# Kernel tuning notes

Measured on AMD Instinct MI355X. Metric: run time of the kernel, lower is better.

Reference implementation:

```python
import jax, jax.numpy as jnp
import numpy as np

K = 16            # number of instance labels (static; labels are 0..K-1)
DELTA_V = 0.2     # delta_variance_loss
DELTA_D = 0.2     # delta_cluster_distance
ALPHA, BETA, GAMMA = 1.0, 1.0, 0.001


def _safe_sqrt(x):
    # sqrt with zero (not nan) gradient at x == 0
    pos = x > 0
    return jnp.where(pos, jnp.sqrt(jnp.where(pos, x, 1.0)), 0.0)


def setup_inputs() -> dict:
    key = jax.random.key(0)
    k1, k2 = jax.random.split(key)
    features = jax.random.normal(k1, (4, 32, 256, 512), dtype=jnp.float32)
    ground_truth = jax.random.randint(k2, (4, 256, 512), 0, K, dtype=jnp.int64)
    return {"features": features, "ground_truth": ground_truth}


def reference(features, ground_truth):
    N, C, H, W = features.shape
    P = H * W
    feat = features.reshape(N, C, P)                  # (N,C,P)
    gt = ground_truth.reshape(N, P)                   # (N,P)
    onehot = (gt[:, :, None] == jnp.arange(K)[None, None, :]).astype(feat.dtype)  # (N,P,K)

    # cluster mean: torch.mean(feature * mask, dim=1) -> masked sum / (H*W)  (faithful quirk)
    mu = jnp.einsum('ncp,npk->nck', feat, onehot) / P  # (N,C,K)

    # ---- variance loss ----
    # per pixel p, instance k: || feat[:,p]*mask_pk - mu[:,k] ||_2 over channels.
    # expand: mask*(||f||^2 - 2 f.mu) + ||mu||^2   (mask in {0,1} so mask^2 = mask)
    sq_f = jnp.sum(feat * feat, axis=1)               # (N,P)
    dot = jnp.einsum('ncp,nck->npk', feat, mu)        # (N,P,K)
    sq_mu = jnp.sum(mu * mu, axis=1)                  # (N,K)
    sq = onehot * (sq_f[:, :, None] - 2.0 * dot) + sq_mu[:, None, :]  # (N,P,K)
    d = _safe_sqrt(jnp.maximum(sq, 0.0))
    v = jnp.mean(d, axis=1)                           # (N,K) mean over pixels
    variance_loss = jnp.mean(jnp.mean(jnp.maximum(v - DELTA_V, 0.0), axis=1))

    # ---- distance loss ----
    gram = jnp.einsum('nck,ncj->nkj', mu, mu)         # (N,K,K)
    sqd = sq_mu[:, :, None] + sq_mu[:, None, :] - 2.0 * gram
    eye = jnp.eye(K, dtype=bool)
    D = jnp.where(eye, 0.0, _safe_sqrt(jnp.maximum(jnp.where(eye, 1.0, sqd), 0.0)))
    mean_dist = jnp.sum(D, axis=2) / (K - 1)          # mean over the K-1 other clusters
    distance_loss = jnp.sum(jnp.maximum(2.0 * DELTA_D - mean_dist, 0.0)) / (N * K)

    # ---- normalization loss ----
    normalization_loss = jnp.mean(jnp.mean(_safe_sqrt(sq_mu), axis=1))

    total_loss = ALPHA * variance_loss + BETA * distance_loss + GAMMA * normalization_loss
    return total_loss, variance_loss, distance_loss, normalization_loss, mu
```

## Files before the change

kernel.cpp:

```cpp
#include <hip/hip_runtime.h>
#include <hip/hip_bf16.h>

#define NIMG 4
#define CCH  32
#define PPIX 131072
#define KLBL 16

#define CPB  4
#define NCG  (CCH / CPB)
#define K1_CHUNK 8192
#define K1_NCHUNK (PPIX / K1_CHUNK)
#define K2_CHUNK 1024
#define K2_NCHUNK (PPIX / K2_CHUNK)


__device__ __forceinline__ float wave_sum(float v) {
#pragma unroll
    for (int m = 1; m < 64; m <<= 1) v += __shfl_xor(v, m);
    return v;
}

__global__ __launch_bounds__(256) void k1_mu(const float* __restrict__ feat,
                                             const int* __restrict__ gt,
                                             float* __restrict__ mu_part) {
    int b     = blockIdx.x;
    int chunk = b % K1_NCHUNK;
    int cg    = (b / K1_NCHUNK) % NCG;
    int n     = b / (K1_NCHUNK * NCG);
    int p0    = chunk * K1_CHUNK;
    int tid   = threadIdx.x;

    const float* f0 = feat + ((size_t)(n * CCH + cg * CPB)) * PPIX + p0;
    const float* f1 = f0 + PPIX;
    const float* f2 = f0 + 2 * (size_t)PPIX;
    const float* f3 = f0 + 3 * (size_t)PPIX;
    const int*   g  = gt + (size_t)n * PPIX + p0;

    float acc0[KLBL], acc1[KLBL], acc2[KLBL], acc3[KLBL];
#pragma unroll
    for (int k = 0; k < KLBL; k++) { acc0[k] = 0.f; acc1[k] = 0.f; acc2[k] = 0.f; acc3[k] = 0.f; }

    for (int i = tid * 4; i < K1_CHUNK; i += 256 * 4) {
        float4 a0 = *(const float4*)(f0 + i);
        float4 a1 = *(const float4*)(f1 + i);
        float4 a2 = *(const float4*)(f2 + i);
        float4 a3 = *(const float4*)(f3 + i);
        int4   l  = *(const int4*)(g + i);
#pragma unroll
        for (int k = 0; k < KLBL; k++) {
            float mx = (l.x == k) ? 1.f : 0.f;
            float my = (l.y == k) ? 1.f : 0.f;
            float mz = (l.z == k) ? 1.f : 0.f;
            float mw = (l.w == k) ? 1.f : 0.f;
            acc0[k] = fmaf(a0.x, mx, acc0[k]); acc0[k] = fmaf(a0.y, my, acc0[k]);
            acc0[k] = fmaf(a0.z, mz, acc0[k]); acc0[k] = fmaf(a0.w, mw, acc0[k]);
            acc1[k] = fmaf(a1.x, mx, acc1[k]); acc1[k] = fmaf(a1.y, my, acc1[k]);
            acc1[k] = fmaf(a1.z, mz, acc1[k]); acc1[k] = fmaf(a1.w, mw, acc1[k]);
            acc2[k] = fmaf(a2.x, mx, acc2[k]); acc2[k] = fmaf(a2.y, my, acc2[k]);
            acc2[k] = fmaf(a2.z, mz, acc2[k]); acc2[k] = fmaf(a2.w, mw, acc2[k]);
            acc3[k] = fmaf(a3.x, mx, acc3[k]); acc3[k] = fmaf(a3.y, my, acc3[k]);
            acc3[k] = fmaf(a3.z, mz, acc3[k]); acc3[k] = fmaf(a3.w, mw, acc3[k]);
        }
    }

    __shared__ float warr[4][64];
    int wave = tid >> 6, lane = tid & 63;
#pragma unroll
    for (int k = 0; k < KLBL; k++) {
        float s0 = wave_sum(acc0[k]);
        float s1 = wave_sum(acc1[k]);
        float s2 = wave_sum(acc2[k]);
        float s3 = wave_sum(acc3[k]);
        if (lane == 0) {
            warr[wave][k]      = s0;
            warr[wave][16 + k] = s1;
            warr[wave][32 + k] = s2;
            warr[wave][48 + k] = s3;
        }
    }
    __syncthreads();
    if (tid < 64) {
        float t = warr[0][tid] + warr[1][tid] + warr[2][tid] + warr[3][tid];
        mu_part[(((size_t)n * K1_NCHUNK + chunk) * NCG + cg) * 64 + tid] = t;
    }
}

__global__ __launch_bounds__(256) void k2_var(const float* __restrict__ feat,
                                              const int* __restrict__ gt,
                                              const float* __restrict__ mu_part,
                                              float* __restrict__ sumd_part,
                                              float* __restrict__ cnt_part) {
    __shared__ float lmu[CCH * KLBL];
    int b     = blockIdx.x;
    int chunk = b % K2_NCHUNK;
    int n     = b / K2_NCHUNK;
    int p0    = chunk * K2_CHUNK;
    int tid   = threadIdx.x;
    const float inv_p = 1.0f / (float)PPIX;

    for (int e = tid; e < CCH * KLBL; e += 256) {
        float s = 0.f;
#pragma unroll
        for (int ch = 0; ch < K1_NCHUNK; ch++)
            s += mu_part[(((size_t)n * K1_NCHUNK + ch) * NCG + (e >> 6)) * 64 + (e & 63)];
        lmu[e] = s * inv_p;
    }
    __syncthreads();

    int p = p0 + tid * 4;
    int4 l = *(const int4*)(gt + (size_t)n * PPIX + p);
    float d2x = 0.f, d2y = 0.f, d2z = 0.f, d2w = 0.f;
    const float* fb = feat + (size_t)n * CCH * PPIX + p;
#pragma unroll 8
    for (int c = 0; c < CCH; c++) {
        float4 f = *(const float4*)(fb + (size_t)c * PPIX);
        float mx = lmu[c * KLBL + l.x];
        float my = lmu[c * KLBL + l.y];
        float mz = lmu[c * KLBL + l.z];
        float mw = lmu[c * KLBL + l.w];
        float ex = f.x - mx, ey = f.y - my, ez = f.z - mz, ew = f.w - mw;
        d2x = fmaf(ex, ex, d2x); d2y = fmaf(ey, ey, d2y);
        d2z = fmaf(ez, ez, d2z); d2w = fmaf(ew, ew, d2w);
    }
    float dx = sqrtf(d2x), dy = sqrtf(d2y), dz = sqrtf(d2z), dw = sqrtf(d2w);

    float s[KLBL], ct[KLBL];
#pragma unroll
    for (int k = 0; k < KLBL; k++) {
        float mx = (l.x == k) ? 1.f : 0.f;
        float my = (l.y == k) ? 1.f : 0.f;
        float mz = (l.z == k) ? 1.f : 0.f;
        float mw = (l.w == k) ? 1.f : 0.f;
        s[k]  = fmaf(dx, mx, fmaf(dy, my, fmaf(dz, mz, dw * mw)));
        ct[k] = mx + my + mz + mw;
    }

    __shared__ float warr[4][32];
    int wave = tid >> 6, lane = tid & 63;
#pragma unroll
    for (int k = 0; k < KLBL; k++) {
        float ssum = wave_sum(s[k]);
        float csum = wave_sum(ct[k]);
        if (lane == 0) { warr[wave][k] = ssum; warr[wave][16 + k] = csum; }
    }
    __syncthreads();
    if (tid < 32) {
        float t = warr[0][tid] + warr[1][tid] + warr[2][tid] + warr[3][tid];
        if (tid < 16) sumd_part[(size_t)b * 16 + tid]        = t;
        else          cnt_part [(size_t)b * 16 + (tid - 16)] = t;
    }
}

__global__ __launch_bounds__(256) void k3_final(const float* __restrict__ mu_part,
                                                const float* __restrict__ sumd_part,
                                                const float* __restrict__ cnt_part,
                                                float* __restrict__ out) {
    __shared__ float mu[NIMG * CCH * KLBL];
    __shared__ float sqmu[NIMG * KLBL];
    __shared__ float ps[4][64], pc[4][64];
    int t = threadIdx.x;
    const float inv_p = 1.0f / (float)PPIX;

    for (int m = t; m < NIMG * CCH * KLBL; m += 256) {
        int n = m >> 9, e = m & 511;
        float s = 0.f;
#pragma unroll
        for (int ch = 0; ch < K1_NCHUNK; ch++)
            s += mu_part[(((size_t)n * K1_NCHUNK + ch) * NCG + (e >> 6)) * 64 + (e & 63)];
        float v = s * inv_p;
        mu[m]      = v;
        out[4 + m] = v;
    }
    __syncthreads();

    float sq = 0.f;
    if (t < 64) {
        int n = t >> 4, k = t & 15;
#pragma unroll
        for (int c = 0; c < CCH; c++) {
            float m = mu[n * 512 + c * KLBL + k];
            sq = fmaf(m, m, sq);
        }
        sqmu[t] = sq;
    }
    {
        int q = t >> 6, nk = t & 63;
        int n2 = nk >> 4, k2 = nk & 15;
        float ss = 0.f, cc = 0.f;
        for (int ch = q * 32; ch < q * 32 + 32; ch++) {
            int idx = (n2 * K2_NCHUNK + ch) * 16 + k2;
            ss += sumd_part[idx];
            cc += cnt_part[idx];
        }
        ps[q][nk] = ss;
        pc[q][nk] = cc;
    }
    __syncthreads();

    if (t < 64) {
        int n = t >> 4, k = t & 15;
        float sumd_t = ps[0][t] + ps[1][t] + ps[2][t] + ps[3][t];
        float cnt_t  = pc[0][t] + pc[1][t] + pc[2][t] + pc[3][t];

        float dsum = 0.f;
#pragma unroll
        for (int j = 0; j < KLBL; j++) {
            if (j == k) continue;
            float gram = 0.f;
#pragma unroll
            for (int c = 0; c < CCH; c++)
                gram = fmaf(mu[n * 512 + c * KLBL + k], mu[n * 512 + c * KLBL + j], gram);
            float sqd = sq + sqmu[n * KLBL + j] - 2.f * gram;
            dsum += (sqd > 0.f) ? sqrtf(sqd) : 0.f;
        }
        float dist_term = fmaxf(2.f * 0.2f - dsum * (1.f / (KLBL - 1)), 0.f);
        float sqm = (sq > 0.f) ? sqrtf(sq) : 0.f;
        float v = (sumd_t + ((float)PPIX - cnt_t) * sqm) * inv_p;
        float var_term = fmaxf(v - 0.2f, 0.f);

        float d_r = wave_sum(dist_term);
        float v_r = wave_sum(var_term);
        float n_r = wave_sum(sqm);
        if (t == 0) {
            float variance_loss      = v_r * (1.f / (NIMG * KLBL));
            float distance_loss      = d_r * (1.f / (NIMG * KLBL));
            float normalization_loss = n_r * (1.f / (NIMG * KLBL));
            out[0] = variance_loss + distance_loss + 0.001f * normalization_loss;
            out[1] = variance_loss;
            out[2] = distance_loss;
            out[3] = normalization_loss;
        }
    }
}

extern "C" void kernel_launch(void* const* d_in, const int* in_sizes, int n_in,
                              void* d_out, int out_size, void* d_ws, size_t ws_size,
                              hipStream_t stream) {
    const float* feat = (const float*)d_in[0];
    const int*   gt   = (const int*)d_in[1];
    float* out       = (float*)d_out;
    float* mu_part   = (float*)d_ws;
    float* sumd_part = mu_part + NIMG * K1_NCHUNK * NCG * 64;
    float* cnt_part  = sumd_part + NIMG * K2_NCHUNK * 16;

    k1_mu<<<NIMG * NCG * K1_NCHUNK, 256, 0, stream>>>(feat, gt, mu_part);
    k2_var<<<NIMG * K2_NCHUNK, 256, 0, stream>>>(feat, gt, mu_part, sumd_part, cnt_part);
    k3_final<<<1, 256, 0, stream>>>(mu_part, sumd_part, cnt_part, out);
}
```

Before: 130.8 us.

## Fuse three kernels into one cooperative kernel with grid-wide syncs

Merges the cluster-mean, variance and final-reduction kernels into a single cooperative kernel separated by grid.sync barriers. The mean is published through the output buffer and reread by block 0 for the final stage. This aims to remove the launch gaps and tail effects between the three dependent kernels. It adds grid-barrier cost and requires all 512 blocks to be co-resident.

```diff
diff --git a/kernel.cpp b/kernel.cpp
--- a/kernel.cpp
+++ b/kernel.cpp
@@ -1,5 +1,8 @@
 #include <hip/hip_runtime.h>
 #include <hip/hip_bf16.h>
+#include <hip/hip_cooperative_groups.h>
+
+namespace cg = cooperative_groups;
 
 #define NIMG 4
 #define CCH  32
@@ -8,10 +11,11 @@
 
 #define CPB  4
 #define NCG  (CCH / CPB)
-#define K1_CHUNK 8192
-#define K1_NCHUNK (PPIX / K1_CHUNK)
-#define K2_CHUNK 1024
-#define K2_NCHUNK (PPIX / K2_CHUNK)
+#define K1_NCHUNK 16
+#define K1_CHUNK  (PPIX / K1_NCHUNK)
+#define K2_NCHUNK 128
+#define K2_CHUNK  (PPIX / K2_NCHUNK)
+#define GRID (NIMG * NCG * K1_NCHUNK)
 
 
 __device__ __forceinline__ float wave_sum(float v) {
@@ -20,215 +24,204 @@
     return v;
 }
 
-__global__ __launch_bounds__(256) void k1_mu(const float* __restrict__ feat,
-                                             const int* __restrict__ gt,
-                                             float* __restrict__ mu_part) {
-    int b     = blockIdx.x;
-    int chunk = b % K1_NCHUNK;
-    int cg    = (b / K1_NCHUNK) % NCG;
-    int n     = b / (K1_NCHUNK * NCG);
-    int p0    = chunk * K1_CHUNK;
-    int tid   = threadIdx.x;
-
-    const float* f0 = feat + ((size_t)(n * CCH + cg * CPB)) * PPIX + p0;
-    const float* f1 = f0 + PPIX;
-    const float* f2 = f0 + 2 * (size_t)PPIX;
-    const float* f3 = f0 + 3 * (size_t)PPIX;
-    const int*   g  = gt + (size_t)n * PPIX + p0;
-
-    float acc0[KLBL], acc1[KLBL], acc2[KLBL], acc3[KLBL];
-#pragma unroll
-    for (int k = 0; k < KLBL; k++) { acc0[k] = 0.f; acc1[k] = 0.f; acc2[k] = 0.f; acc3[k] = 0.f; }
-
-    for (int i = tid * 4; i < K1_CHUNK; i += 256 * 4) {
-        float4 a0 = *(const float4*)(f0 + i);
-        float4 a1 = *(const float4*)(f1 + i);
-        float4 a2 = *(const float4*)(f2 + i);
-        float4 a3 = *(const float4*)(f3 + i);
-        int4   l  = *(const int4*)(g + i);
+__global__ __launch_bounds__(256) void fused_all(const float* __restrict__ feat,
+                                                 const int* __restrict__ gt,
+                                                 float* __restrict__ out,
+                                                 float* __restrict__ ws) {
+    float* mu_part   = ws;
+    float* sumd_part = ws + 32768;
+    float* cnt_part  = sumd_part + 8192;
+
+    cg::grid_group grid = cg::this_grid();
+    const int b    = blockIdx.x;
+    const int tid  = threadIdx.x;
+    const int wave = tid >> 6, lane = tid & 63;
+    const float inv_p = 1.0f / (float)PPIX;
+
+    __shared__ float warr[4][64];
+    __shared__ float lmu[CCH * KLBL];
+    __shared__ float mu3[NIMG * CCH * KLBL];
+    __shared__ float sqmu[NIMG * KLBL];
+    __shared__ float ps[4][64], pc[4][64];
+
+    {
+        int chunk = b % K1_NCHUNK;
+        int cgi   = (b / K1_NCHUNK) % NCG;
+        int n     = b / (K1_NCHUNK * NCG);
+        int p0    = chunk * K1_CHUNK;
+        const float* f0 = feat + ((size_t)(n * CCH + cgi * CPB)) * PPIX + p0;
+        const float* f1 = f0 + PPIX;
+        const float* f2 = f0 + 2 * (size_t)PPIX;
+        const float* f3 = f0 + 3 * (size_t)PPIX;
+        const int*   g  = gt + (size_t)n * PPIX + p0;
+
+        float acc0[KLBL], acc1[KLBL], acc2[KLBL], acc3[KLBL];
+#pragma unroll
+        for (int k = 0; k < KLBL; k++) { acc0[k] = 0.f; acc1[k] = 0.f; acc2[k] = 0.f; acc3[k] = 0.f; }
+
+        for (int i = tid * 4; i < K1_CHUNK; i += 256 * 4) {
+            float4 a0 = *(const float4*)(f0 + i);
+            float4 a1 = *(const float4*)(f1 + i);
+            float4 a2 = *(const float4*)(f2 + i);
+            float4 a3 = *(const float4*)(f3 + i);
+            int4   l  = *(const int4*)(g + i);
+#pragma unroll
+            for (int k = 0; k < KLBL; k++) {
+                float mx = (l.x == k) ? 1.f : 0.f;
+                float my = (l.y == k) ? 1.f : 0.f;
+                float mz = (l.z == k) ? 1.f : 0.f;
+                float mw = (l.w == k) ? 1.f : 0.f;
+                acc0[k] = fmaf(a0.x, mx, acc0[k]); acc0[k] = fmaf(a0.y, my, acc0[k]);
+                acc0[k] = fmaf(a0.z, mz, acc0[k]); acc0[k] = fmaf(a0.w, mw, acc0[k]);
+                acc1[k] = fmaf(a1.x, mx, acc1[k]); acc1[k] = fmaf(a1.y, my, acc1[k]);
+                acc1[k] = fmaf(a1.z, mz, acc1[k]); acc1[k] = fmaf(a1.w, mw, acc1[k]);
+                acc2[k] = fmaf(a2.x, mx, acc2[k]); acc2[k] = fmaf(a2.y, my, acc2[k]);
+                acc2[k] = fmaf(a2.z, mz, acc2[k]); acc2[k] = fmaf(a2.w, mw, acc2[k]);
+                acc3[k] = fmaf(a3.x, mx, acc3[k]); acc3[k] = fmaf(a3.y, my, acc3[k]);
+                acc3[k] = fmaf(a3.z, mz, acc3[k]); acc3[k] = fmaf(a3.w, mw, acc3[k]);
+            }
+        }
+#pragma unroll
+        for (int k = 0; k < KLBL; k++) {
+            float s0 = wave_sum(acc0[k]);
+            float s1 = wave_sum(acc1[k]);
+            float s2 = wave_sum(acc2[k]);
+            float s3 = wave_sum(acc3[k]);
+            if (lane == 0) {
+                warr[wave][k]      = s0;
+                warr[wave][16 + k] = s1;
+                warr[wave][32 + k] = s2;
+                warr[wave][48 + k] = s3;
+            }
+        }
+        __syncthreads();
+        if (tid < 64) {
+            float t = warr[0][tid] + warr[1][tid] + warr[2][tid] + warr[3][tid];
+            mu_part[(((size_t)n * K1_NCHUNK + chunk) * NCG + cgi) * 64 + tid] = t;
+        }
+    }
+    grid.sync();
+
+    {
+        int chunk = b % K2_NCHUNK;
+        int n     = b / K2_NCHUNK;
+        int p0    = chunk * K2_CHUNK;
+
+        for (int e = tid; e < CCH * KLBL; e += 256) {
+            float s = 0.f;
+#pragma unroll
+            for (int ch = 0; ch < K1_NCHUNK; ch++)
+                s += mu_part[(((size_t)n * K1_NCHUNK + ch) * NCG + (e >> 6)) * 64 + (e & 63)];
+            float v = s * inv_p;
+            lmu[e] = v;
+            if (chunk == 0) out[4 + n * 512 + e] = v;
+        }
+        __syncthreads();
+
+        int p = p0 + tid * 4;
+        int4 l = *(const int4*)(gt + (size_t)n * PPIX + p);
+        const float* fb = feat + (size_t)n * CCH * PPIX + p;
+        float d2x = 0.f, d2y = 0.f, d2z = 0.f, d2w = 0.f;
+#pragma unroll 8
+        for (int c = 0; c < CCH; c++) {
+            float4 f = *(const float4*)(fb + (size_t)c * PPIX);
+            float mx = lmu[c * KLBL + l.x];
+            float my = lmu[c * KLBL + l.y];
+            float mz = lmu[c * KLBL + l.z];
+            float mw = lmu[c * KLBL + l.w];
+            float ex = f.x - mx, ey = f.y - my, ez = f.z - mz, ew = f.w - mw;
+            d2x = fmaf(ex, ex, d2x); d2y = fmaf(ey, ey, d2y);
+            d2z = fmaf(ez, ez, d2z); d2w = fmaf(ew, ew, d2w);
+        }
+        float dx = sqrtf(d2x), dy = sqrtf(d2y), dz = sqrtf(d2z), dw = sqrtf(d2w);
+
+        float s[KLBL], ct[KLBL];
 #pragma unroll
         for (int k = 0; k < KLBL; k++) {
             float mx = (l.x == k) ? 1.f : 0.f;
             float my = (l.y == k) ? 1.f : 0.f;
             float mz = (l.z == k) ? 1.f : 0.f;
             float mw = (l.w == k) ? 1.f : 0.f;
-            acc0[k] = fmaf(a0.x, mx, acc0[k]); acc0[k] = fmaf(a0.y, my, acc0[k]);
-            acc0[k] = fmaf(a0.z, mz, acc0[k]); acc0[k] = fmaf(a0.w, mw, acc0[k]);
-            acc1[k] = fmaf(a1.x, mx, acc1[k]); acc1[k] = fmaf(a1.y, my, acc1[k]);
-            acc1[k] = fmaf(a1.z, mz, acc1[k]); acc1[k] = fmaf(a1.w, mw, acc1[k]);
-            acc2[k] = fmaf(a2.x, mx, acc2[k]); acc2[k] = fmaf(a2.y, my, acc2[k]);
-            acc2[k] = fmaf(a2.z, mz, acc2[k]); acc2[k] = fmaf(a2.w, mw, acc2[k]);
-            acc3[k] = fmaf(a3.x, mx, acc3[k]); acc3[k] = fmaf(a3.y, my, acc3[k]);
-            acc3[k] = fmaf(a3.z, mz, acc3[k]); acc3[k] = fmaf(a3.w, mw, acc3[k]);
+            s[k]  = fmaf(dx, mx, fmaf(dy, my, fmaf(dz, mz, dw * mw)));
+            ct[k] = mx + my + mz + mw;
+        }
+#pragma unroll
+        for (int k = 0; k < KLBL; k++) {
+            float ssum = wave_sum(s[k]);
+            float csum = wave_sum(ct[k]);
+            if (lane == 0) { warr[wave][k] = ssum; warr[wave][16 + k] = csum; }
+        }
+        __syncthreads();
+        if (tid < 32) {
+            float t = warr[0][tid] + warr[1][tid] + warr[2][tid] + warr[3][tid];
+            if (tid < 16) sumd_part[(size_t)b * 16 + tid]        = t;
+            else          cnt_part [(size_t)b * 16 + (tid - 16)] = t;
         }
     }
-
-    __shared__ float warr[4][64];
-    int wave = tid >> 6, lane = tid & 63;
-#pragma unroll
-    for (int k = 0; k < KLBL; k++) {
-        float s0 = wave_sum(acc0[k]);
-        float s1 = wave_sum(acc1[k]);
-        float s2 = wave_sum(acc2[k]);
-        float s3 = wave_sum(acc3[k]);
-        if (lane == 0) {
-            warr[wave][k]      = s0;
-            warr[wave][16 + k] = s1;
-            warr[wave][32 + k] = s2;
-            warr[wave][48 + k] = s3;
-        }
-    }
-    __syncthreads();
-    if (tid < 64) {
-        float t = warr[0][tid] + warr[1][tid] + warr[2][tid] + warr[3][tid];
-        mu_part[(((size_t)n * K1_NCHUNK + chunk) * NCG + cg) * 64 + tid] = t;
-    }
-}
-
-__global__ __launch_bounds__(256) void k2_var(const float* __restrict__ feat,
-                                              const int* __restrict__ gt,
-                                              const float* __restrict__ mu_part,
-                                              float* __restrict__ sumd_part,
-                                              float* __restrict__ cnt_part) {
-    __shared__ float lmu[CCH * KLBL];
-    int b     = blockIdx.x;
-    int chunk = b % K2_NCHUNK;
-    int n     = b / K2_NCHUNK;
-    int p0    = chunk * K2_CHUNK;
-    int tid   = threadIdx.x;
-    const float inv_p = 1.0f / (float)PPIX;
-
-    for (int e = tid; e < CCH * KLBL; e += 256) {
-        float s = 0.f;
-#pragma unroll
-        for (int ch = 0; ch < K1_NCHUNK; ch++)
-            s += mu_part[(((size_t)n * K1_NCHUNK + ch) * NCG + (e >> 6)) * 64 + (e & 63)];
-        lmu[e] = s * inv_p;
-    }
-    __syncthreads();
-
-    int p = p0 + tid * 4;
-    int4 l = *(const int4*)(gt + (size_t)n * PPIX + p);
-    float d2x = 0.f, d2y = 0.f, d2z = 0.f, d2w = 0.f;
-    const float* fb = feat + (size_t)n * CCH * PPIX + p;
-#pragma unroll 8
-    for (int c = 0; c < CCH; c++) {
-        float4 f = *(const float4*)(fb + (size_t)c * PPIX);
-        float mx = lmu[c * KLBL + l.x];
-        float my = lmu[c * KLBL + l.y];
-        float mz = lmu[c * KLBL + l.z];
-        float mw = lmu[c * KLBL + l.w];
-        float ex = f.x - mx, ey = f.y - my, ez = f.z - mz, ew = f.w - mw;
-        d2x = fmaf(ex, ex, d2x); d2y = fmaf(ey, ey, d2y);
-        d2z = fmaf(ez, ez, d2z); d2w = fmaf(ew, ew, d2w);
-    }
-    float dx = sqrtf(d2x), dy = sqrtf(d2y), dz = sqrtf(d2z), dw = sqrtf(d2w);
-
-    float s[KLBL], ct[KLBL];
-#pragma unroll
-    for (int k = 0; k < KLBL; k++) {
-        float mx = (l.x == k) ? 1.f : 0.f;
-        float my = (l.y == k) ? 1.f : 0.f;
-        float mz = (l.z == k) ? 1.f : 0.f;
-        float mw = (l.w == k) ? 1.f : 0.f;
-        s[k]  = fmaf(dx, mx, fmaf(dy, my, fmaf(dz, mz, dw * mw)));
-        ct[k] = mx + my + mz + mw;
-    }
-
-    __shared__ float warr[4][32];
-    int wave = tid >> 6, lane = tid & 63;
-#pragma unroll
-    for (int k = 0; k < KLBL; k++) {
-        float ssum = wave_sum(s[k]);
-        float csum = wave_sum(ct[k]);
-        if (lane == 0) { warr[wave][k] = ssum; warr[wave][16 + k] = csum; }
-    }
-    __syncthreads();
-    if (tid < 32) {
-        float t = warr[0][tid] + warr[1][tid] + warr[2][tid] + warr[3][tid];
-        if (tid < 16) sumd_part[(size_t)b * 16 + tid]        = t;
-        else          cnt_part [(size_t)b * 16 + (tid - 16)] = t;
-    }
-}
-
-__global__ __launch_bounds__(256) void k3_final(const float* __restrict__ mu_part,
-                                                const float* __restrict__ sumd_part,
-                                                const float* __restrict__ cnt_part,
-                                                float* __restrict__ out) {
-    __shared__ float mu[NIMG * CCH * KLBL];
-    __shared__ float sqmu[NIMG * KLBL];
-    __shared__ float ps[4][64], pc[4][64];
-    int t = threadIdx.x;
-    const float inv_p = 1.0f / (float)PPIX;
-
-    for (int m = t; m < NIMG * CCH * KLBL; m += 256) {
-        int n = m >> 9, e = m & 511;
-        float s = 0.f;
-#pragma unroll
-        for (int ch = 0; ch < K1_NCHUNK; ch++)
-            s += mu_part[(((size_t)n * K1_NCHUNK + ch) * NCG + (e >> 6)) * 64 + (e & 63)];
-        float v = s * inv_p;
-        mu[m]      = v;
-        out[4 + m] = v;
-    }
-    __syncthreads();
-
-    float sq = 0.f;
-    if (t < 64) {
-        int n = t >> 4, k = t & 15;
-#pragma unroll
-        for (int c = 0; c < CCH; c++) {
-            float m = mu[n * 512 + c * KLBL + k];
-            sq = fmaf(m, m, sq);
-        }
-        sqmu[t] = sq;
-    }
-    {
-        int q = t >> 6, nk = t & 63;
-        int n2 = nk >> 4, k2 = nk & 15;
-        float ss = 0.f, cc = 0.f;
-        for (int ch = q * 32; ch < q * 32 + 32; ch++) {
-            int idx = (n2 * K2_NCHUNK + ch) * 16 + k2;
-            ss += sumd_part[idx];
-            cc += cnt_part[idx];
-        }
-        ps[q][nk] = ss;
-        pc[q][nk] = cc;
-    }
-    __syncthreads();
-
-    if (t < 64) {
-        int n = t >> 4, k = t & 15;
-        float sumd_t = ps[0][t] + ps[1][t] + ps[2][t] + ps[3][t];
-        float cnt_t  = pc[0][t] + pc[1][t] + pc[2][t] + pc[3][t];
-
-        float dsum = 0.f;
-#pragma unroll
-        for (int j = 0; j < KLBL; j++) {
-            if (j == k) continue;
-            float gram = 0.f;
-#pragma unroll
-            for (int c = 0; c < CCH; c++)
-                gram = fmaf(mu[n * 512 + c * KLBL + k], mu[n * 512 + c * KLBL + j], gram);
-            float sqd = sq + sqmu[n * KLBL + j] - 2.f * gram;
-            dsum += (sqd > 0.f) ? sqrtf(sqd) : 0.f;
-        }
-        float dist_term = fmaxf(2.f * 0.2f - dsum * (1.f / (KLBL - 1)), 0.f);
-        float sqm = (sq > 0.f) ? sqrtf(sq) : 0.f;
-        float v = (sumd_t + ((float)PPIX - cnt_t) * sqm) * inv_p;
-        float var_term = fmaxf(v - 0.2f, 0.f);
-
-        float d_r = wave_sum(dist_term);
-        float v_r = wave_sum(var_term);
-        float n_r = wave_sum(sqm);
-        if (t == 0) {
-            float variance_loss      = v_r * (1.f / (NIMG * KLBL));
-            float distance_loss      = d_r * (1.f / (NIMG * KLBL));
-            float normalization_loss = n_r * (1.f / (NIMG * KLBL));
-            out[0] = variance_loss + distance_loss + 0.001f * normalization_loss;
-            out[1] = variance_loss;
-            out[2] = distance_loss;
-            out[3] = normalization_loss;
+    grid.sync();
+
+    if (b == 0) {
+        for (int m = tid; m < NIMG * CCH * KLBL; m += 256)
+            mu3[m] = out[4 + m];
+        __syncthreads();
+
+        float sq = 0.f;
+        if (tid < 64) {
+            int n = tid >> 4, k = tid & 15;
+#pragma unroll
+            for (int c = 0; c < CCH; c++) {
+                float m = mu3[n * 512 + c * KLBL + k];
+                sq = fmaf(m, m, sq);
+            }
+            sqmu[tid] = sq;
+        }
+        {
+            int q = tid >> 6, nk = tid & 63;
+            int n2 = nk >> 4, k2 = nk & 15;
+            float ss = 0.f, cc = 0.f;
+            for (int ch = q * 32; ch < q * 32 + 32; ch++) {
+                int idx = (n2 * K2_NCHUNK + ch) * 16 + k2;
+                ss += sumd_part[idx];
+                cc += cnt_part[idx];
+            }
+            ps[q][nk] = ss;
+            pc[q][nk] = cc;
+        }
+        __syncthreads();
+
+        if (tid < 64) {
+            int n = tid >> 4, k = tid & 15;
+            float sumd_t = ps[0][tid] + ps[1][tid] + ps[2][tid] + ps[3][tid];
+            float cnt_t  = pc[0][tid] + pc[1][tid] + pc[2][tid] + pc[3][tid];
+
+            float dsum = 0.f;
+#pragma unroll
+            for (int j = 0; j < KLBL; j++) {
+                if (j == k) continue;
+                float gram = 0.f;
+#pragma unroll
+                for (int c = 0; c < CCH; c++)
+                    gram = fmaf(mu3[n * 512 + c * KLBL + k], mu3[n * 512 + c * KLBL + j], gram);
+                float sqd = sq + sqmu[n * KLBL + j] - 2.f * gram;
+                dsum += (sqd > 0.f) ? sqrtf(sqd) : 0.f;
+            }
+            float dist_term = fmaxf(2.f * 0.2f - dsum * (1.f / (KLBL - 1)), 0.f);
+            float sqm = (sq > 0.f) ? sqrtf(sq) : 0.f;
+            float v = (sumd_t + ((float)PPIX - cnt_t) * sqm) * inv_p;
+            float var_term = fmaxf(v - 0.2f, 0.f);
+
+            float d_r = wave_sum(dist_term);
+            float v_r = wave_sum(var_term);
+            float n_r = wave_sum(sqm);
+            if (tid == 0) {
+                float variance_loss      = v_r * (1.f / (NIMG * KLBL));
+                float distance_loss      = d_r * (1.f / (NIMG * KLBL));
+                float normalization_loss = n_r * (1.f / (NIMG * KLBL));
+                out[0] = variance_loss + distance_loss + 0.001f * normalization_loss;
+                out[1] = variance_loss;
+                out[2] = distance_loss;
+                out[3] = normalization_loss;
+            }
         }
     }
 }
@@ -238,12 +231,9 @@
                               hipStream_t stream) {
     const float* feat = (const float*)d_in[0];
     const int*   gt   = (const int*)d_in[1];
-    float* out       = (float*)d_out;
-    float* mu_part   = (float*)d_ws;
-    float* sumd_part = mu_part + NIMG * K1_NCHUNK * NCG * 64;
-    float* cnt_part  = sumd_part + NIMG * K2_NCHUNK * 16;
-
-    k1_mu<<<NIMG * NCG * K1_NCHUNK, 256, 0, stream>>>(feat, gt, mu_part);
-    k2_var<<<NIMG * K2_NCHUNK, 256, 0, stream>>>(feat, gt, mu_part, sumd_part, cnt_part);
-    k3_final<<<1, 256, 0, stream>>>(mu_part, sumd_part, cnt_part, out);
+    float*       out  = (float*)d_out;
+    float*       ws   = (float*)d_ws;
+
+    void* args[] = { (void*)&feat, (void*)&gt, (void*)&out, (void*)&ws };
+    hipLaunchCooperativeKernel((void*)fused_all, dim3(GRID), dim3(256), args, 0, stream);
 }
```

New measurement: 215.5 us. 64.8% more time.
